# Kernel tuning notes

Measured on AMD Instinct MI355X. Metric: run time of the kernel, lower is better.

The kernel has to match this reference:

```python
import jax, jax.numpy as jnp
import numpy as np

EPS = 1e-20  # MaskSoftmax epsilon
S, T, B, H, V = 64, 64, 128, 1024, 32000


def _attn(s, h, u, mask, sa_w, sa_b, a1_w, a1_b):
    # Bahdanau attention with mask-softmax over the source (dim 0)
    t = jnp.tanh(s @ sa_w + sa_b + u)               # [S,B,H]
    e = jnp.einsum('sbh,h->sb', t, a1_w) + a1_b     # [S,B]
    x = jnp.exp(e - jnp.max(e, axis=0, keepdims=True)) * mask
    alpha = x / (jnp.sum(x, axis=0, keepdims=True) + EPS)
    return jnp.einsum('sb,sbh->bh', alpha, h)       # [B,H]


def _gru(x, h, ym, W, U, b, C=None, c=None):
    xg = x @ W + b
    if C is not None:
        xg = xg + c @ C
    hg = h @ U
    xz, xr, xh = jnp.split(xg, 3, axis=-1)
    hz, hr, hh = jnp.split(hg, 3, axis=-1)
    z = jax.nn.sigmoid(xz + hz)
    r = jax.nn.sigmoid(xr + hr)
    hn = (1.0 - z) * h + z * jnp.tanh(xh + r * hh)
    m = ym[:, None]
    return m * hn + (1.0 - m) * h


def _forward(ys, xs_h, uh, xs_mask, ys_mask, s_tm1, emb, sa_w, sa_b, a1_w, a1_b,
             ha_w, ha_b, W1, U1, b1, W2, U2, C2, b2,
             ua1_w, ua1_b, ua2_w, ua2_b, ls_w, ls_b, ly_w, ly_b, lc_w, lc_b):
    ys_e = emb[ys]                                              # [T,B,H]
    btg_uh = jnp.einsum('sbh,hk->sbk', xs_h, ha_w) + ha_b        # [S,B,H]

    def step(s, inp):
        y_e, ym = inp
        s_above = _gru(y_e, s, ym, W1, U1, b1)                   # gru1
        a1 = _attn(s_above, xs_h, uh, xs_mask, sa_w, sa_b, a1_w, a1_b)
        a2 = _attn(s_above, xs_h, btg_uh, xs_mask, sa_w, sa_b, a1_w, a1_b)
        s_t = _gru(a1, s_above, ym, W2, U2, b2, C2, a2)          # gru2 with extra ctx
        g = jax.nn.sigmoid(a1 @ ua1_w + ua1_b + a2 @ ua2_w + ua2_b)
        att = g * a1 + (1.0 - g) * a2                            # gated fusion
        logit = s_t @ ls_w + ls_b + y_e @ ly_w + ly_b + att @ lc_w + lc_b  # [B,2H]
        logit = jnp.max(logit.reshape(logit.shape[0], -1, 2), axis=-1)     # maxout
        return s_t, logit

    _, logits = jax.lax.scan(step, s_tm1, (ys_e, ys_mask))       # [T,B,H]
    return logits * ys_mask[:, :, None]


def setup_inputs():
    key = jax.random.key(0)
    ks = jax.random.split(key, 20)
    rn = lambda k, sh, s=0.02: jax.random.normal(k, sh, jnp.float32) * s
    inp = {}
    inp['ys'] = jax.random.randint(ks[0], (T, B), 0, V)
    inp['xs_h'] = jax.random.normal(ks[1], (S, B, H), jnp.float32)
    inp['uh'] = jax.random.normal(ks[2], (S, B, H), jnp.float32)
    inp['xs_mask'] = jnp.ones((S, B), jnp.float32)
    inp['ys_mask'] = jnp.ones((T, B), jnp.float32)
    inp['s_tm1'] = rn(ks[3], (B, H), 1.0)
    emb = rn(ks[4], (V, H), 1.0)
    inp['emb'] = emb.at[0].set(0.0)  # padding_idx = 0
    inp['sa_w'] = rn(ks[5], (H, H)); inp['sa_b'] = jnp.zeros((H,), jnp.float32)
    inp['a1_w'] = rn(ks[6], (H,));   inp['a1_b'] = jnp.zeros((), jnp.float32)
    inp['ha_w'] = rn(ks[7], (H, H)); inp['ha_b'] = jnp.zeros((H,), jnp.float32)
    inp['W1'] = rn(ks[8], (H, 3 * H)); inp['U1'] = rn(ks[9], (H, 3 * H)); inp['b1'] = jnp.zeros((3 * H,), jnp.float32)
    inp['W2'] = rn(ks[10], (H, 3 * H)); inp['U2'] = rn(ks[11], (H, 3 * H)); inp['C2'] = rn(ks[12], (H, 3 * H)); inp['b2'] = jnp.zeros((3 * H,), jnp.float32)
    inp['ua1_w'] = rn(ks[13], (H, H)); inp['ua1_b'] = jnp.zeros((H,), jnp.float32)
    inp['ua2_w'] = rn(ks[14], (H, H)); inp['ua2_b'] = jnp.zeros((H,), jnp.float32)
    inp['ls_w'] = rn(ks[15], (H, 2 * H)); inp['ls_b'] = jnp.zeros((2 * H,), jnp.float32)
    inp['ly_w'] = rn(ks[16], (H, 2 * H)); inp['ly_b'] = jnp.zeros((2 * H,), jnp.float32)
    inp['lc_w'] = rn(ks[17], (H, 2 * H)); inp['lc_b'] = jnp.zeros((2 * H,), jnp.float32)
    return inp


def reference(ys, xs_h, uh, xs_mask, ys_mask, s_tm1, emb, sa_w, sa_b, a1_w, a1_b,
              ha_w, ha_b, W1, U1, b1, W2, U2, C2, b2,
              ua1_w, ua1_b, ua2_w, ua2_b, ls_w, ls_b, ly_w, ly_b, lc_w, lc_b):
    return _forward(ys, xs_h, uh, xs_mask, ys_mask, s_tm1, emb, sa_w, sa_b, a1_w, a1_b,
                    ha_w, ha_b, W1, U1, b1, W2, U2, C2, b2,
                    ua1_w, ua1_b, ua2_w, ua2_b, ls_w, ls_b, ly_w, ly_b, lc_w, lc_b)
```

## Files before the change

### kernel.cpp

```cpp
#include <hip/hip_runtime.h>
#include <hip/hip_bf16.h>
#include <cstddef>
#include <cstdint>

#define Sdim 64
#define Tdim 64
#define Bdim 128
#define Hdim 1024
#define H3 3072
#define TB (Tdim * Bdim)
#define SB (Sdim * Bdim)
#define NWG 256

typedef __attribute__((ext_vector_type(4))) float f32x4;
typedef __attribute__((ext_vector_type(8))) short bf16x8;

__device__ __forceinline__ float rcpf(float x) { return __builtin_amdgcn_rcpf(x); }
__device__ __forceinline__ float sigf(float x) { return rcpf(1.0f + __expf(-x)); }
__device__ __forceinline__ float tanh_fast(float x) {
  x = fminf(fmaxf(x, -15.0f), 15.0f);
  float t = __expf(2.0f * x);
  return (t - 1.0f) * rcpf(t + 1.0f);
}
__device__ __forceinline__ float bl(uint32_t u) { return __uint_as_float(u << 16); }
__device__ __forceinline__ float bh(uint32_t u) { return __uint_as_float(u & 0xffff0000u); }
__device__ __forceinline__ float b2f(uint16_t v) { return __uint_as_float((uint32_t)v << 16); }
__device__ __forceinline__ uint16_t f2b(float f) {
  __hip_bfloat16 h = __float2bfloat16(f);
  return *reinterpret_cast<uint16_t*>(&h);
}

__device__ __forceinline__ uint32_t ald32(const void* p) {
  return __hip_atomic_load((const uint32_t*)p, __ATOMIC_RELAXED, __HIP_MEMORY_SCOPE_AGENT);
}
__device__ __forceinline__ unsigned long long ald64(const void* p) {
  return __hip_atomic_load((const unsigned long long*)p, __ATOMIC_RELAXED, __HIP_MEMORY_SCOPE_AGENT);
}
__device__ __forceinline__ void ast32(void* p, uint32_t v) {
  __hip_atomic_store((uint32_t*)p, v, __ATOMIC_RELAXED, __HIP_MEMORY_SCOPE_AGENT);
}
__device__ __forceinline__ void ast64(void* p, unsigned long long v) {
  __hip_atomic_store((unsigned long long*)p, v, __ATOMIC_RELAXED, __HIP_MEMORY_SCOPE_AGENT);
}
__device__ __forceinline__ float aldf(const void* p) { return __uint_as_float(ald32(p)); }
__device__ __forceinline__ void astf(void* p, float v) { ast32(p, __float_as_uint(v)); }
__device__ __forceinline__ uint4 ald128(const void* p) {
  unsigned long long a = ald64(p);
  unsigned long long b = ald64((const char*)p + 8);
  uint4 r;
  r.x = (uint32_t)a; r.y = (uint32_t)(a >> 32);
  r.z = (uint32_t)b; r.w = (uint32_t)(b >> 32);
  return r;
}

struct MDesc {
  const uint16_t* A0; const uint16_t* B0;
  const uint16_t* A1; const uint16_t* B1;
  const uint16_t* A2; const uint16_t* B2;
  const float* bias0; const float* bias1; const float* bias2;
  float* C;
  int M, N, K;
};

template<int BM, int BN, int MODE>
__global__ __launch_bounds__(256) void mgemm(MDesc d, const float* __restrict__ ymask,
                                             float* __restrict__ outp)
{
  const int nb = blockIdx.x * BN;
  const int mb = blockIdx.y * BM;
  if (nb >= d.N || mb >= d.M) return;

  __shared__ char lds[(BM + BN) * 128];
  char* As = lds;
  char* Bs = lds + BM * 128;

  const int t = threadIdx.x;
  const int lane = t & 63;
  const int wid = t >> 6;
  const int wm = wid >> 1, wn = wid & 1;
  constexpr int WM = BM / 2, WN = BN / 2;
  constexpr int MR = WM / 16, NR = WN / 16;
  constexpr int CA = BM / 32;
  constexpr int CB = BN / 32;

  const int arow_base = wm * WM + (lane & 15);
  const int brow_base = wn * WN + (lane & 15);
  const int akb = (lane >> 4) * 16;
  const int axA = (arow_base & 7) << 4;
  const int axB = (brow_base & 7) << 4;

  f32x4 acc[MR][NR];
  #pragma unroll
  for (int m = 0; m < MR; ++m)
    #pragma unroll
    for (int n = 0; n < NR; ++n)
      acc[m][n] = (f32x4){0.f, 0.f, 0.f, 0.f};

  const int K = d.K;
  const int nkt = K / 64;

  #pragma unroll 1
  for (int p = 0; p < 3; ++p) {
    const uint16_t* A = (p == 0) ? d.A0 : (p == 1 ? d.A1 : d.A2);
    const uint16_t* B = (p == 0) ? d.B0 : (p == 1 ? d.B1 : d.B2);
    if (A == nullptr) break;

    const char* gA[CA]; int lA[CA];
    const char* gB[CB]; int lB[CB];
    #pragma unroll
    for (int c = 0; c < CA; ++c) {
      int i = c * 256 + t, row = i >> 3, kb = (i & 7) * 16;
      gA[c] = (const char*)A + (size_t)(mb + row) * K * 2 + kb;
      lA[c] = row * 128 + (kb ^ ((row & 7) << 4));
    }
    #pragma unroll
    for (int c = 0; c < CB; ++c) {
      int i = c * 256 + t, row = i >> 3, kb = (i & 7) * 16;
      gB[c] = (const char*)B + (size_t)(nb + row) * K * 2 + kb;
      lB[c] = row * 128 + (kb ^ ((row & 7) << 4));
    }

    uint4 ra[CA], rb[CB];
    #pragma unroll
    for (int c = 0; c < CA; ++c) ra[c] = *(const uint4*)gA[c];
    #pragma unroll
    for (int c = 0; c < CB; ++c) rb[c] = *(const uint4*)gB[c];

    for (int kk = 0; kk < nkt; ++kk) {
      __syncthreads();
      #pragma unroll
      for (int c = 0; c < CA; ++c) *(uint4*)(As + lA[c]) = ra[c];
      #pragma unroll
      for (int c = 0; c < CB; ++c) *(uint4*)(Bs + lB[c]) = rb[c];
      __syncthreads();
      if (kk + 1 < nkt) {
        #pragma unroll
        for (int c = 0; c < CA; ++c) ra[c] = *(const uint4*)(gA[c] + (size_t)(kk + 1) * 128);
        #pragma unroll
        for (int c = 0; c < CB; ++c) rb[c] = *(const uint4*)(gB[c] + (size_t)(kk + 1) * 128);
      }
      #pragma unroll
      for (int ks = 0; ks < 2; ++ks) {
        bf16x8 av[MR], bv[NR];
        #pragma unroll
        for (int m = 0; m < MR; ++m) {
          int row = arow_base + m * 16;
          av[m] = *(const bf16x8*)(As + row * 128 + ((ks * 64 + akb) ^ axA));
        }
        #pragma unroll
        for (int n = 0; n < NR; ++n) {
          int row = brow_base + n * 16;
          bv[n] = *(const bf16x8*)(Bs + row * 128 + ((ks * 64 + akb) ^ axB));
        }
        #pragma unroll
        for (int m = 0; m < MR; ++m)
          #pragma unroll
          for (int n = 0; n < NR; ++n)
            acc[m][n] = __builtin_amdgcn_mfma_f32_16x16x32_bf16(av[m], bv[n], acc[m][n], 0, 0, 0);
      }
    }
  }

  const int cm = (lane >> 4) * 4;
  const int cn = lane & 15;
  #pragma unroll
  for (int n = 0; n < NR; ++n) {
    int col = nb + wn * WN + n * 16 + cn;
    float bias = 0.f;
    if (d.bias0) bias += d.bias0[col];
    if (d.bias1) bias += d.bias1[col];
    if (d.bias2) bias += d.bias2[col];
    #pragma unroll
    for (int m = 0; m < MR; ++m) {
      #pragma unroll
      for (int j = 0; j < 4; ++j) {
        int row = mb + wm * WM + m * 16 + cm + j;
        float v = acc[m][n][j] + bias;
        if (MODE == 1) {
          ((uint16_t*)d.C)[(size_t)row * d.N + col] = f2b(v);
        } else {
          float o = __shfl_xor(v, 1);
          if (!(lane & 1))
            outp[(size_t)row * (d.N / 2) + (col >> 1)] = fmaxf(v, o) * ymask[row];
        }
      }
    }
  }
}

static inline MDesc mk(const uint16_t* A0, const uint16_t* B0,
                       const uint16_t* A1, const uint16_t* B1,
                       const uint16_t* A2, const uint16_t* B2,
                       const float* b0, const float* b1, const float* b2,
                       float* C, int M, int N, int K)
{
  MDesc d;
  d.A0 = A0; d.B0 = B0; d.A1 = A1; d.B1 = B1; d.A2 = A2; d.B2 = B2;
  d.bias0 = b0; d.bias1 = b1; d.bias2 = b2;
  d.C = C; d.M = M; d.N = N; d.K = K;
  return d;
}

__global__ __launch_bounds__(256) void transpose_bf16_k(const float* __restrict__ in,
                                                        uint16_t* __restrict__ out,
                                                        int K, int N)
{
  __shared__ float tile[32][33];
  int nx = blockIdx.x * 32, ky = blockIdx.y * 32;
  int tx = threadIdx.x & 31, ty = threadIdx.x >> 5;
  #pragma unroll
  for (int i = 0; i < 4; ++i)
    tile[ty + i * 8][tx] = in[(size_t)(ky + ty + i * 8) * N + nx + tx];
  __syncthreads();
  #pragma unroll
  for (int i = 0; i < 4; ++i)
    out[(size_t)(nx + ty + i * 8) * K + ky + tx] = f2b(tile[tx][ty + i * 8]);
}

__global__ __launch_bounds__(256) void ptranspose_k(const float* __restrict__ in,
                                                    uint16_t* __restrict__ out,
                                                    int K, int N)
{
  __shared__ float tile[32][33];
  int nx = blockIdx.x * 32, ky = blockIdx.y * 32;
  int tx = threadIdx.x & 31, ty = threadIdx.x >> 5;
  #pragma unroll
  for (int i = 0; i < 4; ++i)
    tile[ty + i * 8][tx] = in[(size_t)(ky + ty + i * 8) * N + nx + tx];
  __syncthreads();
  #pragma unroll
  for (int i = 0; i < 4; ++i) {
    int n = nx + ty + i * 8;
    int h = n & 1023, g = n >> 10;
    int np = (h >> 4) * 48 + g * 16 + (h & 15);
    out[(size_t)np * K + ky + tx] = f2b(tile[tx][ty + i * 8]);
  }
}

__global__ __launch_bounds__(256) void pack_k(const float* __restrict__ b1,
                                              const float* __restrict__ b2,
                                              float* __restrict__ b1p,
                                              float* __restrict__ b2p,
                                              int* __restrict__ bar)
{
  int i = blockIdx.x * 256 + threadIdx.x;
  if (i < 1024) bar[i] = 0;
  if (i < H3) {
    int g = (i >> 4) % 3, hblk = i / 48, hi = i & 15;
    int n = g * 1024 + hblk * 16 + hi;
    b1p[i] = b1[n];
    b2p[i] = b2[n];
  }
}

__global__ __launch_bounds__(256) void cvt_bf16_k(const float* __restrict__ in,
                                                  uint16_t* __restrict__ out)
{
  int gid = blockIdx.x * 256 + threadIdx.x;
  float4 v = ((const float4*)in)[gid];
  uint2 o;
  o.x = (uint32_t)f2b(v.x) | ((uint32_t)f2b(v.y) << 16);
  o.y = (uint32_t)f2b(v.z) | ((uint32_t)f2b(v.w) << 16);
  ((uint2*)out)[gid] = o;
}

__global__ __launch_bounds__(256) void embed_k(const int* __restrict__ ys,
                                               const float* __restrict__ emb,
                                               uint16_t* __restrict__ ys_e)
{
  int gid = blockIdx.x * 256 + threadIdx.x;
  int h4 = gid & 255;
  int tb = gid >> 8;
  int tok = ys[tb];
  float4 v = ((const float4*)emb)[(size_t)tok * 256 + h4];
  uint2 o;
  o.x = (uint32_t)f2b(v.x) | ((uint32_t)f2b(v.y) << 16);
  o.y = (uint32_t)f2b(v.z) | ((uint32_t)f2b(v.w) << 16);
  ((uint2*)ys_e)[gid] = o;
}

struct ScanArgs {
  const uint16_t *U1p, *W2p, *C2p, *U2p;
  const uint16_t *sawt, *ua1t, *ua2t;
  const uint16_t *xw1p;
  const uint16_t *uh_bf, *btg_bf, *xs_bf;
  const uint16_t *stm1_bf;
  const float *s_tm1, *ys_mask, *xs_mask, *a1w, *a1b, *sa_b;
  const float *b2p, *ua1_b, *ua2_b;
  float *sf0, *sf1, *sab_f, *qbuf, *e1, *e2, *c1f, *c2f, *ahg;
  uint16_t *sab_bf, *c1b, *c2b, *shist_bf, *att_bf;
  int *bar;
};

__device__ __forceinline__ void gsync(int* bar, int gen, int wg) {
  __syncthreads();
  if (threadIdx.x == 0) {
    asm volatile("s_waitcnt vmcnt(0)" ::: "memory");
    int old = __hip_atomic_fetch_add(bar + (wg & 15) * 32, 1,
                                     __ATOMIC_RELAXED, __HIP_MEMORY_SCOPE_AGENT);
    if (old == gen * 16 - 1) {
      int ro = __hip_atomic_fetch_add(bar + 512, 1,
                                      __ATOMIC_RELAXED, __HIP_MEMORY_SCOPE_AGENT);
      if (ro == gen * 16 - 1)
        __hip_atomic_store(bar + 544, gen, __ATOMIC_RELAXED, __HIP_MEMORY_SCOPE_AGENT);
    }
    while (__hip_atomic_load(bar + 544, __ATOMIC_RELAXED, __HIP_MEMORY_SCOPE_AGENT) < gen)
      __builtin_amdgcn_s_sleep(2);
    asm volatile("s_waitcnt vmcnt(0)" ::: "memory");
  }
  __syncthreads();
}

#define DUMP_OFF (368 * 128)

__global__ __launch_bounds__(256, 1) void scan2_k(ScanArgs a) {
  const int wg = blockIdx.x;
  const int t = threadIdx.x;
  const int lane = t & 63, w = t >> 6;
  const int r15 = lane & 15;
  const int akb = (lane >> 4) * 16;
  __shared__ char lds[48 * 1024];
  int gen = 0;

  float wv[16];
  {
    const float* wp = a.a1w + lane * 16;
    #pragma unroll
    for (int j = 0; j < 16; ++j) wv[j] = wp[j];
  }
  const float abv = a.a1b[0];

  const int b34 = wg & 127;
  const uint16_t* src34 = (wg < 128) ? a.uh_bf : a.btg_bf;
  const size_t s34_base = ((size_t)(w * 16) * Bdim + b34) * 1024 + lane * 16;
  float* cf34 = (wg < 128) ? a.c1f : a.c2f;
  uint16_t* cb34 = (wg < 128) ? a.c1b : a.c2b;
  const uint16_t* xp34 = a.xs_bf + (size_t)b34 * 1024 + t * 4;

  const int bh6 = (wg & 127) >> 6, hb6 = wg & 63;
  const char* ga6[4]; int la6[4];
  {
    #pragma unroll
    for (int c = 0; c < 4; ++c) {
      int i = c * 256 + t;
      if (i < 512) {
        int row = i >> 3, kb = (i & 7) * 16;
        ga6[c] = (const char*)a.sab_bf + ((size_t)(bh6 * 64 + row) * 1024) * 2 + kb;
        la6[c] = row * 128 + (kb ^ ((row & 7) << 4));
      } else if (i < 896) {
        int j2 = i - 512, row = j2 >> 3, kb = (j2 & 7) * 16;
        ga6[c] = (const char*)a.U2p + ((size_t)(hb6 * 48 + row) * 1024) * 2 + kb;
        la6[c] = (64 + row) * 128 + (kb ^ ((row & 7) << 4));
      } else {
        ga6[c] = (const char*)a.U2p; la6[c] = DUMP_OFF;
      }
    }
  }

  const int bh5 = (wg & 127) >> 6, hblk = wg & 63;
  const char* ga5[8]; int la5[8];
  {
    #pragma unroll
    for (int c = 0; c < 8; ++c) {
      int i = c * 256 + t;
      int kb = (i & 7) * 16, grow = i >> 3;
      const char* gp;
      if (grow < 64)       gp = (const char*)a.c1b  + ((size_t)(bh5 * 64 + grow)        * 1024) * 2;
      else if (grow < 128) gp = (const char*)a.c2b  + ((size_t)(bh5 * 64 + grow - 64)   * 1024) * 2;
      else if (grow < 176) gp = (const char*)a.W2p  + ((size_t)(hblk * 48 + grow - 128) * 1024) * 2;
      else if (grow < 224) gp = (const char*)a.C2p  + ((size_t)(hblk * 48 + grow - 176) * 1024) * 2;
      else if (grow < 240) gp = (const char*)a.ua1t + ((size_t)(hblk * 16 + grow - 224) * 1024) * 2;
      else                 gp = (const char*)a.ua2t + ((size_t)(hblk * 16 + grow - 240) * 1024) * 2;
      ga5[c] = gp + kb;
      la5[c] = grow * 128 + (kb ^ ((grow & 7) << 4));
    }
  }

  for (int step = 0; step < Tdim; ++step) {
    const uint16_t* sprev_bf = step ? (a.shist_bf + (size_t)(step - 1) * Bdim * Hdim) : a.stm1_bf;
    const float* sprev_f = (step == 0) ? a.s_tm1 : ((step & 1) ? a.sf0 : a.sf1);
    float* snext_f = (step & 1) ? a.sf1 : a.sf0;
    const float* ymt = a.ys_mask + (size_t)step * Bdim;
    uint16_t* shist_t = a.shist_bf + (size_t)step * Bdim * Hdim;
    uint16_t* att_t = a.att_bf + (size_t)step * Bdim * Hdim;
    const uint16_t* xw1t = a.xw1p + (size_t)step * Bdim * H3;

    uint4 v6w2, v6w3;

    if (wg < 128) {
      const char* ga1[4]; int la1[4];
      #pragma unroll
      for (int c = 0; c < 4; ++c) {
        int i = c * 256 + t;
        if (i < 512) {
          int row = i >> 3, kb = (i & 7) * 16;
          ga1[c] = (const char*)sprev_bf + ((size_t)(bh5 * 64 + row) * 1024) * 2 + kb;
          la1[c] = row * 128 + (kb ^ ((row & 7) << 4));
        } else if (i < 896) {
          int j2 = i - 512, row = j2 >> 3, kb = (j2 & 7) * 16;
          ga1[c] = (const char*)a.U1p + ((size_t)(hblk * 48 + row) * 1024) * 2 + kb;
          la1[c] = (64 + row) * 128 + (kb ^ ((row & 7) << 4));
        } else {
          ga1[c] = (const char*)a.U1p;
          la1[c] = DUMP_OFF;
        }
      }
      f32x4 ac0 = {0.f,0.f,0.f,0.f}, ac1 = ac0, ac2 = ac0;
      uint4 v1[4];
      #pragma unroll
      for (int c = 0; c < 4; ++c)
        v1[c] = (c < 2) ? ald128(ga1[c]) : *(const uint4*)ga1[c];
      const int arow = w * 16 + r15;
      const int axA = (arow & 7) << 4;
      const int axB = (r15 & 7) << 4;
      for (int kk = 0; kk < 16; ++kk) {
        __syncthreads();
        #pragma unroll
        for (int c = 0; c < 4; ++c) *(uint4*)(lds + la1[c]) = v1[c];
        __syncthreads();
        if (kk < 15) {
          #pragma unroll
          for (int c = 0; c < 4; ++c)
            v1[c] = (c < 2) ? ald128(ga1[c] + (size_t)(kk + 1) * 128)
                            : *(const uint4*)(ga1[c] + (size_t)(kk + 1) * 128);
        }
        #pragma unroll
        for (int ks = 0; ks < 2; ++ks) {
          int ko = ks * 64 + akb;
          bf16x8 av = *(const bf16x8*)(lds + arow * 128 + (ko ^ axA));
          bf16x8 b0 = *(const bf16x8*)(lds + (64 + r15) * 128 + (ko ^ axB));
          bf16x8 b1 = *(const bf16x8*)(lds + (80 + r15) * 128 + (ko ^ axB));
          bf16x8 b2 = *(const bf16x8*)(lds + (96 + r15) * 128 + (ko ^ axB));
          ac0 = __builtin_amdgcn_mfma_f32_16x16x32_bf16(av, b0, ac0, 0, 0, 0);
          ac1 = __builtin_amdgcn_mfma_f32_16x16x32_bf16(av, b1, ac1, 0, 0, 0);
          ac2 = __builtin_amdgcn_mfma_f32_16x16x32_bf16(av, b2, ac2, 0, 0, 0);
        }
      }
      const int hgl = hblk * 16 + r15;
      const int bbase = bh5 * 64 + w * 16 + ((lane >> 4) << 2);
      #pragma unroll
      for (int j = 0; j < 4; ++j) {
        int b = bbase + j;
        size_t xr_ = (size_t)b * H3 + hblk * 48 + r15;
        float xz = b2f(xw1t[xr_]);
        float xr = b2f(xw1t[xr_ + 16]);
        float xh = b2f(xw1t[xr_ + 32]);
        float hp = aldf(sprev_f + b * 1024 + hgl);
        float z = sigf(xz + ac0[j]);
        float r = sigf(xr + ac1[j]);
        float hn = (1.f - z) * hp + z * tanh_fast(xh + r * ac2[j]);
        float m = ymt[b];
        float o = m * hn + (1.f - m) * hp;
        astf(a.sab_f + b * 1024 + hgl, o);
        uint32_t me = f2b(o);
        uint32_t other = (uint32_t)__shfl_xor((int)me, 1);
        if (!(lane & 1))
          ast32((char*)a.sab_bf + ((size_t)b * 1024 + hgl) * 2, me | (other << 16));
      }
    } else {
      v6w2 = *(const uint4*)ga6[2];
      v6w3 = *(const uint4*)ga6[3];
    }
    gsync(a.bar, ++gen, wg);

    if (wg < 64) {
      const int bh2 = wg >> 5, nblk = wg & 31;
      const char* ga2[3]; int la2[3];
      #pragma unroll
      for (int c = 0; c < 3; ++c) {
        int i = c * 256 + t;
        if (i < 512) {
          int row = i >> 3, kb = (i & 7) * 16;
          ga2[c] = (const char*)a.sab_bf + ((size_t)(bh2 * 64 + row) * 1024) * 2 + kb;
          la2[c] = row * 128 + (kb ^ ((row & 7) << 4));
        } else {
          int j2 = i - 512, row = j2 >> 3, kb = (j2 & 7) * 16;
          ga2[c] = (const char*)a.sawt + ((size_t)(nblk * 32 + row) * 1024) * 2 + kb;
          la2[c] = (64 + row) * 128 + (kb ^ ((row & 7) << 4));
        }
      }
      f32x4 q0 = {0.f,0.f,0.f,0.f}, q1 = q0;
      uint4 v2[3];
      #pragma unroll
      for (int c = 0; c < 3; ++c)
        v2[c] = (c < 2) ? ald128(ga2[c]) : *(const uint4*)ga2[c];
      const int arow = w * 16 + r15;
      const int axA = (arow & 7) << 4;
      const int axB = (r15 & 7) << 4;
      for (int kk = 0; kk < 16; ++kk) {
        __syncthreads();
        #pragma unroll
        for (int c = 0; c < 3; ++c) *(uint4*)(lds + la2[c]) = v2[c];
        __syncthreads();
        if (kk < 15) {
          #pragma unroll
          for (int c = 0; c < 3; ++c)
            v2[c] = (c < 2) ? ald128(ga2[c] + (size_t)(kk + 1) * 128)
                            : *(const uint4*)(ga2[c] + (size_t)(kk + 1) * 128);
        }
        #pragma unroll
        for (int ks = 0; ks < 2; ++ks) {
          int ko = ks * 64 + akb;
          bf16x8 av = *(const bf16x8*)(lds + arow * 128 + (ko ^ axA));
          bf16x8 b0 = *(const bf16x8*)(lds + (64 + r15) * 128 + (ko ^ axB));
          bf16x8 b1 = *(const bf16x8*)(lds + (80 + r15) * 128 + (ko ^ axB));
          q0 = __builtin_amdgcn_mfma_f32_16x16x32_bf16(av, b0, q0, 0, 0, 0);
          q1 = __builtin_amdgcn_mfma_f32_16x16x32_bf16(av, b1, q1, 0, 0, 0);
        }
      }
      #pragma unroll
      for (int n = 0; n < 2; ++n) {
        int col = nblk * 32 + n * 16 + r15;
        float sb = a.sa_b[col];
        #pragma unroll
        for (int j = 0; j < 4; ++j) {
          int b = bh2 * 64 + w * 16 + ((lane >> 4) << 2) + j;
          astf(a.qbuf + b * 1024 + col, (n ? q1[j] : q0[j]) + sb);
        }
      }
    } else if (wg >= 128) {
      f32x4 ac0 = {0.f,0.f,0.f,0.f}, ac1 = ac0, ac2 = ac0;
      uint4 vU[4];
      vU[0] = ald128(ga6[0]); vU[1] = ald128(ga6[1]);
      vU[2] = v6w2; vU[3] = v6w3;
      const int arow = w * 16 + r15;
      const int axA = (arow & 7) << 4;
      const int axB = (r15 & 7) << 4;
      for (int kk = 0; kk < 16; ++kk) {
        __syncthreads();
        #pragma unroll
        for (int c = 0; c < 4; ++c) *(uint4*)(lds + la6[c]) = vU[c];
        __syncthreads();
        if (kk < 15) {
          #pragma unroll
          for (int c = 0; c < 4; ++c)
            vU[c] = (c < 2) ? ald128(ga6[c] + (size_t)(kk + 1) * 128)
                            : *(const uint4*)(ga6[c] + (size_t)(kk + 1) * 128);
        }
        #pragma unroll
        for (int ks = 0; ks < 2; ++ks) {
          int ko = ks * 64 + akb;
          bf16x8 av = *(const bf16x8*)(lds + arow * 128 + (ko ^ axA));
          bf16x8 b0 = *(const bf16x8*)(lds + (64 + r15) * 128 + (ko ^ axB));
          bf16x8 b1 = *(const bf16x8*)(lds + (80 + r15) * 128 + (ko ^ axB));
          bf16x8 b2 = *(const bf16x8*)(lds + (96 + r15) * 128 + (ko ^ axB));
          ac0 = __builtin_amdgcn_mfma_f32_16x16x32_bf16(av, b0, ac0, 0, 0, 0);
          ac1 = __builtin_amdgcn_mfma_f32_16x16x32_bf16(av, b1, ac1, 0, 0, 0);
          ac2 = __builtin_amdgcn_mfma_f32_16x16x32_bf16(av, b2, ac2, 0, 0, 0);
        }
      }
      const int bbase6 = bh6 * 64 + w * 16 + ((lane >> 4) << 2);
      #pragma unroll
      for (int j = 0; j < 4; ++j) {
        int b = bbase6 + j;
        float* ap = a.ahg + (size_t)b * H3 + hb6 * 48 + r15;
        astf(ap, ac0[j]);
        astf(ap + 16, ac1[j]);
        astf(ap + 32, ac2[j]);
      }
    }
    uint4 px0 = *(const uint4*)(src34 + s34_base);
    uint4 px1 = *(const uint4*)(src34 + s34_base + 8);
    gsync(a.bar, ++gen, wg);

    {
      float* e_lds = (float*)lds;
      float qv[16];
      const float* qp = a.qbuf + (size_t)b34 * 1024 + lane * 16;
      #pragma unroll
      for (int k2 = 0; k2 < 8; ++k2) {
        unsigned long long q2 = ald64(qp + k2 * 2);
        qv[2 * k2]     = __uint_as_float((uint32_t)q2);
        qv[2 * k2 + 1] = __uint_as_float((uint32_t)(q2 >> 32));
      }
      #pragma unroll 1
      for (int si = 0; si < 16; ++si) {
        uint4 u0 = px0, u1 = px1;
        if (si < 15) {
          const uint16_t* np = src34 + s34_base + (size_t)(si + 1) * Bdim * 1024;
          px0 = *(const uint4*)np;
          px1 = *(const uint4*)(np + 8);
        }
        float pv = 0.f;
        uint32_t uu[8] = {u0.x,u0.y,u0.z,u0.w,u1.x,u1.y,u1.z,u1.w};
        #pragma unroll
        for (int k = 0; k < 8; ++k) {
          pv += wv[2*k]   * tanh_fast(qv[2*k]   + bl(uu[k]));
          pv += wv[2*k+1] * tanh_fast(qv[2*k+1] + bh(uu[k]));
        }
        #pragma unroll
        for (int off = 32; off > 0; off >>= 1) pv += __shfl_xor(pv, off);
        if (lane == 0) e_lds[w * 16 + si] = pv + abv;
      }
      __syncthreads();
      if (w == 0) {
        float vv = e_lds[lane];
        float mx = vv;
        #pragma unroll
        for (int off = 32; off > 0; off >>= 1) mx = fmaxf(mx, __shfl_xor(mx, off));
        float x = __expf(vv - mx) * a.xs_mask[lane * Bdim + b34];
        float sm = x;
        #pragma unroll
        for (int off = 32; off > 0; off >>= 1) sm += __shfl_xor(sm, off);
        e_lds[lane] = x * rcpf(sm + 1e-20f);
      }
      __syncthreads();
      float s0 = 0.f, s1 = 0.f, s2 = 0.f, s3 = 0.f;
      #pragma unroll 8
      for (int s = 0; s < Sdim; ++s) {
        unsigned long long u = *(const unsigned long long*)(xp34 + (size_t)s * Bdim * 1024);
        float aa = e_lds[s];
        s0 += aa * bl((uint32_t)u);
        s1 += aa * bh((uint32_t)u);
        s2 += aa * bl((uint32_t)(u >> 32));
        s3 += aa * bh((uint32_t)(u >> 32));
      }
      size_t o = (size_t)b34 * 1024 + t * 4;
      ast64(cf34 + o,     (unsigned long long)__float_as_uint(s0)
                        | ((unsigned long long)__float_as_uint(s1) << 32));
      ast64(cf34 + o + 2, (unsigned long long)__float_as_uint(s2)
                        | ((unsigned long long)__float_as_uint(s3) << 32));
      unsigned long long pb = (unsigned long long)f2b(s0)
                            | ((unsigned long long)f2b(s1) << 16)
                            | ((unsigned long long)f2b(s2) << 32)
                            | ((unsigned long long)f2b(s3) << 48);
      ast64((char*)cb34 + o * 2, pb);
    }
    uint4 v5[8];
    if (wg < 128) {
      #pragma unroll
      for (int c = 4; c < 8; ++c) v5[c] = *(const uint4*)ga5[c];
    }
    gsync(a.bar, ++gen, wg);

    if (wg < 128) {
      #pragma unroll
      for (int c = 0; c < 4; ++c) v5[c] = ald128(ga5[c]);
      f32x4 ax0 = {0.f,0.f,0.f,0.f}, ax1 = ax0, ax2 = ax0, ag = ax0;
      for (int kk = 0; kk < 16; ++kk) {
        __syncthreads();
        #pragma unroll
        for (int c = 0; c < 8; ++c) *(uint4*)(lds + la5[c]) = v5[c];
        __syncthreads();
        if (kk < 15) {
          #pragma unroll
          for (int c = 0; c < 8; ++c)
            v5[c] = (c < 4) ? ald128(ga5[c] + (size_t)(kk + 1) * 128)
                            : *(const uint4*)(ga5[c] + (size_t)(kk + 1) * 128);
        }
        #pragma unroll
        for (int ks = 0; ks < 2; ++ks) {
          const int ko = ks * 64 + akb;
          #define LD(row_) (*(const bf16x8*)(lds + (row_) * 128 + (ko ^ (((row_) & 7) << 4))))
          bf16x8 a1v = LD(w * 16 + r15);
          bf16x8 a2v = LD(64 + w * 16 + r15);
          bf16x8 bw0 = LD(128 + r15), bw1 = LD(144 + r15), bw2 = LD(160 + r15);
          bf16x8 bc0 = LD(176 + r15), bc1 = LD(192 + r15), bc2 = LD(208 + r15);
          bf16x8 g1v = LD(224 + r15), g2v = LD(240 + r15);
          #undef LD
          ax0 = __builtin_amdgcn_mfma_f32_16x16x32_bf16(a1v, bw0, ax0, 0, 0, 0);
          ax0 = __builtin_amdgcn_mfma_f32_16x16x32_bf16(a2v, bc0, ax0, 0, 0, 0);
          ax1 = __builtin_amdgcn_mfma_f32_16x16x32_bf16(a1v, bw1, ax1, 0, 0, 0);
          ax1 = __builtin_amdgcn_mfma_f32_16x16x32_bf16(a2v, bc1, ax1, 0, 0, 0);
          ax2 = __builtin_amdgcn_mfma_f32_16x16x32_bf16(a1v, bw2, ax2, 0, 0, 0);
          ax2 = __builtin_amdgcn_mfma_f32_16x16x32_bf16(a2v, bc2, ax2, 0, 0, 0);
          ag  = __builtin_amdgcn_mfma_f32_16x16x32_bf16(a1v, g1v, ag, 0, 0, 0);
          ag  = __builtin_amdgcn_mfma_f32_16x16x32_bf16(a2v, g2v, ag, 0, 0, 0);
        }
      }
      const int hgl = hblk * 16 + r15;
      float bz  = a.b2p[hblk * 48 + r15];
      float brr = a.b2p[hblk * 48 + 16 + r15];
      float bhh = a.b2p[hblk * 48 + 32 + r15];
      float gb  = a.ua1_b[hgl] + a.ua2_b[hgl];
      const int bbase = bh5 * 64 + w * 16 + ((lane >> 4) << 2);
      float ahz[4], ahr[4], ahh[4], hpv[4], c1v[4], c2v[4];
      #pragma unroll
      for (int j = 0; j < 4; ++j) {
        int b = bbase + j;
        const float* ap = a.ahg + (size_t)b * H3 + hblk * 48 + r15;
        ahz[j] = aldf(ap);
        ahr[j] = aldf(ap + 16);
        ahh[j] = aldf(ap + 32);
        hpv[j] = aldf(a.sab_f + (size_t)b * 1024 + hgl);
        c1v[j] = aldf(a.c1f + (size_t)b * 1024 + hgl);
        c2v[j] = aldf(a.c2f + (size_t)b * 1024 + hgl);
      }
      #pragma unroll
      for (int j = 0; j < 4; ++j) {
        int b = bbase + j;
        float hp = hpv[j];
        float z = sigf(ax0[j] + bz + ahz[j]);
        float r = sigf(ax1[j] + brr + ahr[j]);
        float hn = (1.f - z) * hp + z * tanh_fast(ax2[j] + bhh + r * ahh[j]);
        float m = ymt[b];
        float st = m * hn + (1.f - m) * hp;
        astf(snext_f + b * 1024 + hgl, st);
        uint32_t me = f2b(st);
        uint32_t other = (uint32_t)__shfl_xor((int)me, 1);
        if (!(lane & 1))
          ast32((char*)shist_t + ((size_t)b * 1024 + hgl) * 2, me | (other << 16));
        float g = sigf(ag[j] + gb);
        float att = g * c1v[j] + (1.f - g) * c2v[j];
        att_t[(size_t)b * 1024 + hgl] = f2b(att);
      }
    }
    gsync(a.bar, ++gen, wg);
  }
}

extern "C" void kernel_launch(void* const* d_in, const int* in_sizes, int n_in,
                              void* d_out, int out_size, void* d_ws, size_t ws_size,
                              hipStream_t stream)
{
  const int*   ys      = (const int*)  d_in[0];
  const float* xs_h    = (const float*)d_in[1];
  const float* uh      = (const float*)d_in[2];
  const float* xs_mask = (const float*)d_in[3];
  const float* ys_mask = (const float*)d_in[4];
  const float* s_tm1   = (const float*)d_in[5];
  const float* emb     = (const float*)d_in[6];
  const float* sa_w    = (const float*)d_in[7];
  const float* sa_b    = (const float*)d_in[8];
  const float* a1_w    = (const float*)d_in[9];
  const float* a1_b    = (const float*)d_in[10];
  const float* ha_w    = (const float*)d_in[11];
  const float* ha_b    = (const float*)d_in[12];
  const float* W1      = (const float*)d_in[13];
  const float* U1      = (const float*)d_in[14];
  const float* b1      = (const float*)d_in[15];
  const float* W2      = (const float*)d_in[16];
  const float* U2      = (const float*)d_in[17];
  const float* C2      = (const float*)d_in[18];
  const float* b2      = (const float*)d_in[19];
  const float* ua1_w   = (const float*)d_in[20];
  const float* ua1_b   = (const float*)d_in[21];
  const float* ua2_w   = (const float*)d_in[22];
  const float* ua2_b   = (const float*)d_in[23];
  const float* ls_w    = (const float*)d_in[24];
  const float* ls_b    = (const float*)d_in[25];
  const float* ly_w    = (const float*)d_in[26];
  const float* ly_b    = (const float*)d_in[27];
  const float* lc_w    = (const float*)d_in[28];
  const float* lc_b    = (const float*)d_in[29];
  (void)in_sizes; (void)n_in; (void)out_size; (void)ws_size;

  float* out = (float*)d_out;

  char* wp = (char*)d_ws;
  auto alloc = [&](size_t bytes) { char* r = wp; wp += (bytes + 255) & ~(size_t)255; return r; };

  uint16_t* W1p  = (uint16_t*)alloc((size_t)H3 * Hdim * 2);
  uint16_t* U1p  = (uint16_t*)alloc((size_t)H3 * Hdim * 2);
  uint16_t* W2p  = (uint16_t*)alloc((size_t)H3 * Hdim * 2);
  uint16_t* U2p  = (uint16_t*)alloc((size_t)H3 * Hdim * 2);
  uint16_t* C2p  = (uint16_t*)alloc((size_t)H3 * Hdim * 2);
  uint16_t* sawt = (uint16_t*)alloc((size_t)Hdim * Hdim * 2);
  uint16_t* hawt = (uint16_t*)alloc((size_t)Hdim * Hdim * 2);
  uint16_t* ua1t = (uint16_t*)alloc((size_t)Hdim * Hdim * 2);
  uint16_t* ua2t = (uint16_t*)alloc((size_t)Hdim * Hdim * 2);
  uint16_t* lst  = (uint16_t*)alloc((size_t)2048 * Hdim * 2);
  uint16_t* lyt  = (uint16_t*)alloc((size_t)2048 * Hdim * 2);
  uint16_t* lct  = (uint16_t*)alloc((size_t)2048 * Hdim * 2);
  float* b1p = (float*)alloc((size_t)H3 * 4);
  float* b2p = (float*)alloc((size_t)H3 * 4);
  int* bar   = (int*)alloc(4096);
  uint16_t* uh_bf   = (uint16_t*)alloc((size_t)SB * Hdim * 2);
  uint16_t* xs_bf   = (uint16_t*)alloc((size_t)SB * Hdim * 2);
  uint16_t* btg_bf  = (uint16_t*)alloc((size_t)SB * Hdim * 2);
  uint16_t* ys_e_bf = (uint16_t*)alloc((size_t)TB * Hdim * 2);
  uint16_t* xw1p    = (uint16_t*)alloc((size_t)TB * H3 * 2);
  uint16_t* shist_bf= (uint16_t*)alloc((size_t)TB * Hdim * 2);
  uint16_t* att_bf  = (uint16_t*)alloc((size_t)TB * Hdim * 2);
  uint16_t* stm1_bf = (uint16_t*)alloc((size_t)Bdim * Hdim * 2);
  float* sab_f = (float*)alloc((size_t)Bdim * Hdim * 4);
  uint16_t* sab_bf = (uint16_t*)alloc((size_t)Bdim * Hdim * 2);
  float* qbuf = (float*)alloc((size_t)Bdim * Hdim * 4);
  float* c1f  = (float*)alloc((size_t)Bdim * Hdim * 4);
  float* c2f  = (float*)alloc((size_t)Bdim * Hdim * 4);
  uint16_t* c1b = (uint16_t*)alloc((size_t)Bdim * Hdim * 2);
  uint16_t* c2b = (uint16_t*)alloc((size_t)Bdim * Hdim * 2);
  float* e1 = (float*)alloc((size_t)SB * 4);
  float* e2 = (float*)alloc((size_t)SB * 4);
  float* sf0 = (float*)alloc((size_t)Bdim * Hdim * 4);
  float* sf1 = (float*)alloc((size_t)Bdim * Hdim * 4);
  float* ahg = (float*)alloc((size_t)Bdim * H3 * 4);

  pack_k<<<12, 256, 0, stream>>>(b1, b2, b1p, b2p, bar);

  auto ptr3 = [&](const float* in, uint16_t* o) {
    ptranspose_k<<<dim3(H3 / 32, Hdim / 32), 256, 0, stream>>>(in, o, Hdim, H3);
  };
  ptr3(W1, W1p); ptr3(U1, U1p); ptr3(W2, W2p); ptr3(U2, U2p); ptr3(C2, C2p);

  auto tr = [&](const float* in, uint16_t* o, int K, int N) {
    transpose_bf16_k<<<dim3(N / 32, K / 32), 256, 0, stream>>>(in, o, K, N);
  };
  tr(sa_w, sawt, Hdim, Hdim); tr(ha_w, hawt, Hdim, Hdim);
  tr(ua1_w, ua1t, Hdim, Hdim); tr(ua2_w, ua2t, Hdim, Hdim);
  tr(ls_w, lst, Hdim, 2048); tr(ly_w, lyt, Hdim, 2048); tr(lc_w, lct, Hdim, 2048);

  cvt_bf16_k<<<(SB * Hdim / 4) / 256, 256, 0, stream>>>(uh, uh_bf);
  cvt_bf16_k<<<(SB * Hdim / 4) / 256, 256, 0, stream>>>(xs_h, xs_bf);
  cvt_bf16_k<<<(Bdim * Hdim / 4) / 256, 256, 0, stream>>>(s_tm1, stm1_bf);
  embed_k<<<(TB * Hdim / 4) / 256, 256, 0, stream>>>(ys, emb, ys_e_bf);

  {
    MDesc d = mk(ys_e_bf, W1p, 0, 0, 0, 0, b1p, 0, 0, (float*)xw1p, TB, H3, Hdim);
    mgemm<128, 128, 1><<<dim3(H3 / 128, TB / 128), 256, 0, stream>>>(d, nullptr, nullptr);
  }
  {
    MDesc d = mk(xs_bf, hawt, 0, 0, 0, 0, ha_b, 0, 0, (float*)btg_bf, SB, Hdim, Hdim);
    mgemm<128, 128, 1><<<dim3(Hdim / 128, SB / 128), 256, 0, stream>>>(d, nullptr, nullptr);
  }

  ScanArgs sa;
  sa.U1p = U1p; sa.W2p = W2p; sa.C2p = C2p; sa.U2p = U2p;
  sa.sawt = sawt; sa.ua1t = ua1t; sa.ua2t = ua2t;
  sa.xw1p = xw1p;
  sa.uh_bf = uh_bf; sa.btg_bf = btg_bf; sa.xs_bf = xs_bf;
  sa.stm1_bf = stm1_bf;
  sa.s_tm1 = s_tm1; sa.ys_mask = ys_mask; sa.xs_mask = xs_mask;
  sa.a1w = a1_w; sa.a1b = a1_b; sa.sa_b = sa_b;
  sa.b2p = b2p; sa.ua1_b = ua1_b; sa.ua2_b = ua2_b;
  sa.sf0 = sf0; sa.sf1 = sf1; sa.sab_f = sab_f; sa.qbuf = qbuf;
  sa.e1 = e1; sa.e2 = e2; sa.c1f = c1f; sa.c2f = c2f; sa.ahg = ahg;
  sa.sab_bf = sab_bf; sa.c1b = c1b; sa.c2b = c2b;
  sa.shist_bf = shist_bf; sa.att_bf = att_bf;
  sa.bar = bar;
  scan2_k<<<NWG, 256, 0, stream>>>(sa);

  {
    MDesc d = mk(shist_bf, lst, ys_e_bf, lyt, att_bf, lct, ls_b, ly_b, lc_b,
                 nullptr, TB, 2048, Hdim);
    mgemm<128, 128, 2><<<dim3(2048 / 128, TB / 128), 256, 0, stream>>>(d, ys_mask, out);
  }
}
```

Measured before the change: 5.473 ms.

## Double-buffer LDS tiles and prefetch two K-tiles ahead in scan GEMM loops

```diff
diff --git a/kernel.cpp b/kernel.cpp
--- a/kernel.cpp
+++ b/kernel.cpp
@@ -311,7 +311,10 @@
   __syncthreads();
 }
 
-#define DUMP_OFF (368 * 128)
+#define HS1 16384
+#define HS2 12288
+#define HS6 16384
+#define HS5 32768
 
 __global__ __launch_bounds__(256, 1) void scan2_k(ScanArgs a) {
   const int wg = blockIdx.x;
@@ -319,7 +322,7 @@
   const int lane = t & 63, w = t >> 6;
   const int r15 = lane & 15;
   const int akb = (lane >> 4) * 16;
-  __shared__ char lds[48 * 1024];
+  __shared__ char lds[64 * 1024];
   int gen = 0;
 
   float wv[16];
@@ -343,17 +346,17 @@
     #pragma unroll
     for (int c = 0; c < 4; ++c) {
       int i = c * 256 + t;
+      int row = i >> 3, kb = (i & 7) * 16;
       if (i < 512) {
-        int row = i >> 3, kb = (i & 7) * 16;
         ga6[c] = (const char*)a.sab_bf + ((size_t)(bh6 * 64 + row) * 1024) * 2 + kb;
-        la6[c] = row * 128 + (kb ^ ((row & 7) << 4));
       } else if (i < 896) {
-        int j2 = i - 512, row = j2 >> 3, kb = (j2 & 7) * 16;
-        ga6[c] = (const char*)a.U2p + ((size_t)(hb6 * 48 + row) * 1024) * 2 + kb;
-        la6[c] = (64 + row) * 128 + (kb ^ ((row & 7) << 4));
+        int j2 = i - 512; int row2 = j2 >> 3;
+        ga6[c] = (const char*)a.U2p + ((size_t)(hb6 * 48 + row2) * 1024) * 2 + kb;
+        row = 64 + row2;
       } else {
-        ga6[c] = (const char*)a.U2p; la6[c] = DUMP_OFF;
-      }
+        ga6[c] = (const char*)a.U2p + kb;
+      }
+      la6[c] = row * 128 + (kb ^ ((row & 7) << 4));
     }
   }
 
@@ -385,56 +388,66 @@
     uint16_t* att_t = a.att_bf + (size_t)step * Bdim * Hdim;
     const uint16_t* xw1t = a.xw1p + (size_t)step * Bdim * H3;
 
-    uint4 v6w2, v6w3;
+    uint4 v6w0, v6w1, v6w2, v6w3;
 
     if (wg < 128) {
       const char* ga1[4]; int la1[4];
       #pragma unroll
       for (int c = 0; c < 4; ++c) {
         int i = c * 256 + t;
+        int row = i >> 3, kb = (i & 7) * 16;
         if (i < 512) {
-          int row = i >> 3, kb = (i & 7) * 16;
           ga1[c] = (const char*)sprev_bf + ((size_t)(bh5 * 64 + row) * 1024) * 2 + kb;
-          la1[c] = row * 128 + (kb ^ ((row & 7) << 4));
         } else if (i < 896) {
-          int j2 = i - 512, row = j2 >> 3, kb = (j2 & 7) * 16;
-          ga1[c] = (const char*)a.U1p + ((size_t)(hblk * 48 + row) * 1024) * 2 + kb;
-          la1[c] = (64 + row) * 128 + (kb ^ ((row & 7) << 4));
+          int j2 = i - 512; int row2 = j2 >> 3;
+          ga1[c] = (const char*)a.U1p + ((size_t)(hblk * 48 + row2) * 1024) * 2 + kb;
+          row = 64 + row2;
         } else {
-          ga1[c] = (const char*)a.U1p;
-          la1[c] = DUMP_OFF;
-        }
+          ga1[c] = (const char*)a.U1p + kb;
+        }
+        la1[c] = row * 128 + (kb ^ ((row & 7) << 4));
       }
       f32x4 ac0 = {0.f,0.f,0.f,0.f}, ac1 = ac0, ac2 = ac0;
-      uint4 v1[4];
-      #pragma unroll
-      for (int c = 0; c < 4; ++c)
-        v1[c] = (c < 2) ? ald128(ga1[c]) : *(const uint4*)ga1[c];
       const int arow = w * 16 + r15;
       const int axA = (arow & 7) << 4;
       const int axB = (r15 & 7) << 4;
-      for (int kk = 0; kk < 16; ++kk) {
-        __syncthreads();
-        #pragma unroll
-        for (int c = 0; c < 4; ++c) *(uint4*)(lds + la1[c]) = v1[c];
-        __syncthreads();
-        if (kk < 15) {
-          #pragma unroll
-          for (int c = 0; c < 4; ++c)
-            v1[c] = (c < 2) ? ald128(ga1[c] + (size_t)(kk + 1) * 128)
-                            : *(const uint4*)(ga1[c] + (size_t)(kk + 1) * 128);
-        }
+      uint4 rA[4], rB[4];
+      auto ld1 = [&](uint4* r, int tile) {
+        #pragma unroll
+        for (int c = 0; c < 4; ++c)
+          r[c] = (c < 2) ? ald128(ga1[c] + (size_t)tile * 128)
+                         : *(const uint4*)(ga1[c] + (size_t)tile * 128);
+      };
+      auto st1 = [&](const uint4* r, int half) {
+        char* base = lds + half * HS1;
+        #pragma unroll
+        for (int c = 0; c < 4; ++c) *(uint4*)(base + la1[c]) = r[c];
+      };
+      auto cp1 = [&](int half) {
+        const char* base = lds + half * HS1;
         #pragma unroll
         for (int ks = 0; ks < 2; ++ks) {
           int ko = ks * 64 + akb;
-          bf16x8 av = *(const bf16x8*)(lds + arow * 128 + (ko ^ axA));
-          bf16x8 b0 = *(const bf16x8*)(lds + (64 + r15) * 128 + (ko ^ axB));
-          bf16x8 b1 = *(const bf16x8*)(lds + (80 + r15) * 128 + (ko ^ axB));
-          bf16x8 b2 = *(const bf16x8*)(lds + (96 + r15) * 128 + (ko ^ axB));
+          bf16x8 av = *(const bf16x8*)(base + arow * 128 + (ko ^ axA));
+          bf16x8 b0 = *(const bf16x8*)(base + (64 + r15) * 128 + (ko ^ axB));
+          bf16x8 b1 = *(const bf16x8*)(base + (80 + r15) * 128 + (ko ^ axB));
+          bf16x8 b2 = *(const bf16x8*)(base + (96 + r15) * 128 + (ko ^ axB));
           ac0 = __builtin_amdgcn_mfma_f32_16x16x32_bf16(av, b0, ac0, 0, 0, 0);
           ac1 = __builtin_amdgcn_mfma_f32_16x16x32_bf16(av, b1, ac1, 0, 0, 0);
           ac2 = __builtin_amdgcn_mfma_f32_16x16x32_bf16(av, b2, ac2, 0, 0, 0);
         }
+      };
+      ld1(rA, 0); ld1(rB, 1);
+      st1(rA, 0);
+      #pragma unroll 1
+      for (int kk2 = 0; kk2 < 8; ++kk2) {
+        __syncthreads();
+        st1(rB, 1);
+        if (kk2 < 7) ld1(rA, 2 * kk2 + 2);
+        cp1(0);
+        __syncthreads();
+        if (kk2 < 7) { st1(rA, 0); ld1(rB, 2 * kk2 + 3); }
+        cp1(1);
       }
       const int hgl = hblk * 16 + r15;
       const int bbase = bh5 * 64 + w * 16 + ((lane >> 4) << 2);
@@ -458,8 +471,10 @@
           ast32((char*)a.sab_bf + ((size_t)b * 1024 + hgl) * 2, me | (other << 16));
       }
     } else {
-      v6w2 = *(const uint4*)ga6[2];
-      v6w3 = *(const uint4*)ga6[3];
+      v6w0 = *(const uint4*)ga6[2];
+      v6w1 = *(const uint4*)ga6[3];
+      v6w2 = *(const uint4*)(ga6[2] + 128);
+      v6w3 = *(const uint4*)(ga6[3] + 128);
     }
     gsync(a.bar, ++gen, wg);
 
@@ -469,44 +484,56 @@
       #pragma unroll
       for (int c = 0; c < 3; ++c) {
         int i = c * 256 + t;
+        int row, kb = (i & 7) * 16;
         if (i < 512) {
-          int row = i >> 3, kb = (i & 7) * 16;
+          row = i >> 3;
           ga2[c] = (const char*)a.sab_bf + ((size_t)(bh2 * 64 + row) * 1024) * 2 + kb;
-          la2[c] = row * 128 + (kb ^ ((row & 7) << 4));
         } else {
-          int j2 = i - 512, row = j2 >> 3, kb = (j2 & 7) * 16;
-          ga2[c] = (const char*)a.sawt + ((size_t)(nblk * 32 + row) * 1024) * 2 + kb;
-          la2[c] = (64 + row) * 128 + (kb ^ ((row & 7) << 4));
-        }
+          int j2 = i - 512; int row2 = j2 >> 3;
+          ga2[c] = (const char*)a.sawt + ((size_t)(nblk * 32 + row2) * 1024) * 2 + kb;
+          row = 64 + row2;
+        }
+        la2[c] = row * 128 + (kb ^ ((row & 7) << 4));
       }
       f32x4 q0 = {0.f,0.f,0.f,0.f}, q1 = q0;
-      uint4 v2[3];
-      #pragma unroll
-      for (int c = 0; c < 3; ++c)
-        v2[c] = (c < 2) ? ald128(ga2[c]) : *(const uint4*)ga2[c];
       const int arow = w * 16 + r15;
       const int axA = (arow & 7) << 4;
       const int axB = (r15 & 7) << 4;
-      for (int kk = 0; kk < 16; ++kk) {
-        __syncthreads();
-        #pragma unroll
-        for (int c = 0; c < 3; ++c) *(uint4*)(lds + la2[c]) = v2[c];
-        __syncthreads();
-        if (kk < 15) {
-          #pragma unroll
-          for (int c = 0; c < 3; ++c)
-            v2[c] = (c < 2) ? ald128(ga2[c] + (size_t)(kk + 1) * 128)
-                            : *(const uint4*)(ga2[c] + (size_t)(kk + 1) * 128);
-        }
+      uint4 rA[3], rB[3];
+      auto ld2 = [&](uint4* r, int tile) {
+        #pragma unroll
+        for (int c = 0; c < 3; ++c)
+          r[c] = (c < 2) ? ald128(ga2[c] + (size_t)tile * 128)
+                         : *(const uint4*)(ga2[c] + (size_t)tile * 128);
+      };
+      auto st2 = [&](const uint4* r, int half) {
+        char* base = lds + half * HS2;
+        #pragma unroll
+        for (int c = 0; c < 3; ++c) *(uint4*)(base + la2[c]) = r[c];
+      };
+      auto cp2 = [&](int half) {
+        const char* base = lds + half * HS2;
         #pragma unroll
         for (int ks = 0; ks < 2; ++ks) {
           int ko = ks * 64 + akb;
-          bf16x8 av = *(const bf16x8*)(lds + arow * 128 + (ko ^ axA));
-          bf16x8 b0 = *(const bf16x8*)(lds + (64 + r15) * 128 + (ko ^ axB));
-          bf16x8 b1 = *(const bf16x8*)(lds + (80 + r15) * 128 + (ko ^ axB));
+          bf16x8 av = *(const bf16x8*)(base + arow * 128 + (ko ^ axA));
+          bf16x8 b0 = *(const bf16x8*)(base + (64 + r15) * 128 + (ko ^ axB));
+          bf16x8 b1 = *(const bf16x8*)(base + (80 + r15) * 128 + (ko ^ axB));
           q0 = __builtin_amdgcn_mfma_f32_16x16x32_bf16(av, b0, q0, 0, 0, 0);
           q1 = __builtin_amdgcn_mfma_f32_16x16x32_bf16(av, b1, q1, 0, 0, 0);
         }
+      };
+      ld2(rA, 0); ld2(rB, 1);
+      st2(rA, 0);
+      #pragma unroll 1
+      for (int kk2 = 0; kk2 < 8; ++kk2) {
+        __syncthreads();
+        st2(rB, 1);
+        if (kk2 < 7) ld2(rA, 2 * kk2 + 2);
+        cp2(0);
+        __syncthreads();
+        if (kk2 < 7) { st2(rA, 0); ld2(rB, 2 * kk2 + 3); }
+        cp2(1);
       }
       #pragma unroll
       for (int n = 0; n < 2; ++n) {
@@ -520,34 +547,49 @@
       }
     } else if (wg >= 128) {
       f32x4 ac0 = {0.f,0.f,0.f,0.f}, ac1 = ac0, ac2 = ac0;
-      uint4 vU[4];
-      vU[0] = ald128(ga6[0]); vU[1] = ald128(ga6[1]);
-      vU[2] = v6w2; vU[3] = v6w3;
       const int arow = w * 16 + r15;
       const int axA = (arow & 7) << 4;
       const int axB = (r15 & 7) << 4;
-      for (int kk = 0; kk < 16; ++kk) {
-        __syncthreads();
-        #pragma unroll
-        for (int c = 0; c < 4; ++c) *(uint4*)(lds + la6[c]) = vU[c];
-        __syncthreads();
-        if (kk < 15) {
-          #pragma unroll
-          for (int c = 0; c < 4; ++c)
-            vU[c] = (c < 2) ? ald128(ga6[c] + (size_t)(kk + 1) * 128)
-                            : *(const uint4*)(ga6[c] + (size_t)(kk + 1) * 128);
-        }
+      uint4 rA[4], rB[4];
+      auto ld6 = [&](uint4* r, int tile) {
+        #pragma unroll
+        for (int c = 0; c < 4; ++c)
+          r[c] = (c < 2) ? ald128(ga6[c] + (size_t)tile * 128)
+                         : *(const uint4*)(ga6[c] + (size_t)tile * 128);
+      };
+      auto st6 = [&](const uint4* r, int half) {
+        char* base = lds + half * HS6;
+        #pragma unroll
+        for (int c = 0; c < 4; ++c) *(uint4*)(base + la6[c]) = r[c];
+      };
+      auto cp6 = [&](int half) {
+        const char* base = lds + half * HS6;
         #pragma unroll
         for (int ks = 0; ks < 2; ++ks) {
           int ko = ks * 64 + akb;
-          bf16x8 av = *(const bf16x8*)(lds + arow * 128 + (ko ^ axA));
-          bf16x8 b0 = *(const bf16x8*)(lds + (64 + r15) * 128 + (ko ^ axB));
-          bf16x8 b1 = *(const bf16x8*)(lds + (80 + r15) * 128 + (ko ^ axB));
-          bf16x8 b2 = *(const bf16x8*)(lds + (96 + r15) * 128 + (ko ^ axB));
+          bf16x8 av = *(const bf16x8*)(base + arow * 128 + (ko ^ axA));
+          bf16x8 b0 = *(const bf16x8*)(base + (64 + r15) * 128 + (ko ^ axB));
+          bf16x8 b1 = *(const bf16x8*)(base + (80 + r15) * 128 + (ko ^ axB));
+          bf16x8 b2 = *(const bf16x8*)(base + (96 + r15) * 128 + (ko ^ axB));
           ac0 = __builtin_amdgcn_mfma_f32_16x16x32_bf16(av, b0, ac0, 0, 0, 0);
           ac1 = __builtin_amdgcn_mfma_f32_16x16x32_bf16(av, b1, ac1, 0, 0, 0);
           ac2 = __builtin_amdgcn_mfma_f32_16x16x32_bf16(av, b2, ac2, 0, 0, 0);
         }
+      };
+      rA[0] = ald128(ga6[0]);       rA[1] = ald128(ga6[1]);
+      rA[2] = v6w0;                 rA[3] = v6w1;
+      rB[0] = ald128(ga6[0] + 128); rB[1] = ald128(ga6[1] + 128);
+      rB[2] = v6w2;                 rB[3] = v6w3;
+      st6(rA, 0);
+      #pragma unroll 1
+      for (int kk2 = 0; kk2 < 8; ++kk2) {
+        __syncthreads();
+        st6(rB, 1);
+        if (kk2 < 7) ld6(rA, 2 * kk2 + 2);
+        cp6(0);
+        __syncthreads();
+        if (kk2 < 7) { st6(rA, 0); ld6(rB, 2 * kk2 + 3); }
+        cp6(1);
       }
       const int bbase6 = bh6 * 64 + w * 16 + ((lane >> 4) << 2);
       #pragma unroll
@@ -559,8 +601,8 @@
         astf(ap + 32, ac2[j]);
       }
     }
-    uint4 px0 = *(const uint4*)(src34 + s34_base);
-    uint4 px1 = *(const uint4*)(src34 + s34_base + 8);
+    uint4 pa0 = *(const uint4*)(src34 + s34_base);
+    uint4 pa1 = *(const uint4*)(src34 + s34_base + 8);
     gsync(a.bar, ++gen, wg);
 
     {
@@ -573,14 +615,7 @@
         qv[2 * k2]     = __uint_as_float((uint32_t)q2);
         qv[2 * k2 + 1] = __uint_as_float((uint32_t)(q2 >> 32));
       }
-      #pragma unroll 1
-      for (int si = 0; si < 16; ++si) {
-        uint4 u0 = px0, u1 = px1;
-        if (si < 15) {
-          const uint16_t* np = src34 + s34_base + (size_t)(si + 1) * Bdim * 1024;
-          px0 = *(const uint4*)np;
-          px1 = *(const uint4*)(np + 8);
-        }
+      auto score = [&](uint4 u0, uint4 u1, int si) {
         float pv = 0.f;
         uint32_t uu[8] = {u0.x,u0.y,u0.z,u0.w,u1.x,u1.y,u1.z,u1.w};
         #pragma unroll
@@ -591,6 +626,32 @@
         #pragma unroll
         for (int off = 32; off > 0; off >>= 1) pv += __shfl_xor(pv, off);
         if (lane == 0) e_lds[w * 16 + si] = pv + abv;
+      };
+      uint4 pb0, pb1;
+      {
+        const uint16_t* np = src34 + s34_base + (size_t)Bdim * 1024;
+        pb0 = *(const uint4*)np; pb1 = *(const uint4*)(np + 8);
+      }
+      #pragma unroll 1
+      for (int s2 = 0; s2 < 8; ++s2) {
+        {
+          int si = 2 * s2;
+          uint4 u0 = pa0, u1 = pa1;
+          if (s2 < 7) {
+            const uint16_t* np = src34 + s34_base + (size_t)(si + 2) * Bdim * 1024;
+            pa0 = *(const uint4*)np; pa1 = *(const uint4*)(np + 8);
+          }
+          score(u0, u1, si);
+        }
+        {
+          int si = 2 * s2 + 1;
+          uint4 u0 = pb0, u1 = pb1;
+          if (s2 < 7) {
+            const uint16_t* np = src34 + s34_base + (size_t)(si + 2) * Bdim * 1024;
+            pb0 = *(const uint4*)np; pb1 = *(const uint4*)(np + 8);
+          }
+          score(u0, u1, si);
+        }
       }
       __syncthreads();
       if (w == 0) {
@@ -626,32 +687,36 @@
                             | ((unsigned long long)f2b(s3) << 48);
       ast64((char*)cb34 + o * 2, pb);
     }
-    uint4 v5[8];
+    uint4 v5w[8];
     if (wg < 128) {
       #pragma unroll
-      for (int c = 4; c < 8; ++c) v5[c] = *(const uint4*)ga5[c];
+      for (int c = 4; c < 8; ++c) {
+        v5w[c - 4] = *(const uint4*)ga5[c];
+        v5w[c]     = *(const uint4*)(ga5[c] + 128);
+      }
     }
     gsync(a.bar, ++gen, wg);
 
     if (wg < 128) {
-      #pragma unroll
-      for (int c = 0; c < 4; ++c) v5[c] = ald128(ga5[c]);
       f32x4 ax0 = {0.f,0.f,0.f,0.f}, ax1 = ax0, ax2 = ax0, ag = ax0;
-      for (int kk = 0; kk < 16; ++kk) {
-        __syncthreads();
-        #pragma unroll
-        for (int c = 0; c < 8; ++c) *(uint4*)(lds + la5[c]) = v5[c];
-        __syncthreads();
-        if (kk < 15) {
-          #pragma unroll
-          for (int c = 0; c < 8; ++c)
-            v5[c] = (c < 4) ? ald128(ga5[c] + (size_t)(kk + 1) * 128)
-                            : *(const uint4*)(ga5[c] + (size_t)(kk + 1) * 128);
-        }
+      uint4 rA[8], rB[8];
+      auto ld5 = [&](uint4* r, int tile) {
+        #pragma unroll
+        for (int c = 0; c < 8; ++c)
+          r[c] = (c < 4) ? ald128(ga5[c] + (size_t)tile * 128)
+                         : *(const uint4*)(ga5[c] + (size_t)tile * 128);
+      };
+      auto st5 = [&](const uint4* r, int half) {
+        char* base = lds + half * HS5;
+        #pragma unroll
+        for (int c = 0; c < 8; ++c) *(uint4*)(base + la5[c]) = r[c];
+      };
+      auto cp5 = [&](int half) {
+        const char* base = lds + half * HS5;
         #pragma unroll
         for (int ks = 0; ks < 2; ++ks) {
           const int ko = ks * 64 + akb;
-          #define LD(row_) (*(const bf16x8*)(lds + (row_) * 128 + (ko ^ (((row_) & 7) << 4))))
+          #define LD(row_) (*(const bf16x8*)(base + (row_) * 128 + (ko ^ (((row_) & 7) << 4))))
           bf16x8 a1v = LD(w * 16 + r15);
           bf16x8 a2v = LD(64 + w * 16 + r15);
           bf16x8 bw0 = LD(128 + r15), bw1 = LD(144 + r15), bw2 = LD(160 + r15);
@@ -667,6 +732,24 @@
           ag  = __builtin_amdgcn_mfma_f32_16x16x32_bf16(a1v, g1v, ag, 0, 0, 0);
           ag  = __builtin_amdgcn_mfma_f32_16x16x32_bf16(a2v, g2v, ag, 0, 0, 0);
         }
+      };
+      #pragma unroll
+      for (int c = 0; c < 4; ++c) {
+        rA[c] = ald128(ga5[c]);
+        rB[c] = ald128(ga5[c] + 128);
+      }
+      #pragma unroll
+      for (int c = 4; c < 8; ++c) { rA[c] = v5w[c - 4]; rB[c] = v5w[c]; }
+      st5(rA, 0);
+      #pragma unroll 1
+      for (int kk2 = 0; kk2 < 8; ++kk2) {
+        __syncthreads();
+        st5(rB, 1);
+        if (kk2 < 7) ld5(rA, 2 * kk2 + 2);
+        cp5(0);
+        __syncthreads();
+        if (kk2 < 7) { st5(rA, 0); ld5(rB, 2 * kk2 + 3); }
+        cp5(1);
       }
       const int hgl = hblk * 16 + r15;
       float bz  = a.b2p[hblk * 48 + r15];
```

After: 5.119 ms. 1.07x faster.
